# Performance work log

Measured on AMD Instinct MI355X. Metric: run time of the kernel, lower is better.

## Reference

```python
import jax, jax.numpy as jnp
import numpy as np

B, N, D = 32, 2048, 320

def _init(key, shape, fan_in):
    return jax.random.normal(key, shape, dtype=jnp.float32) / np.sqrt(fan_in).astype(np.float32)

def setup_inputs() -> dict:
    key = jax.random.key(0)
    ks = jax.random.split(key, 11)
    return {
        "x": jax.random.normal(ks[0], (B, N, D), dtype=jnp.float32),
        # downs MLP: 320->160->80
        "W1": _init(ks[1], (320, 160), 320), "b1": jnp.zeros((160,), jnp.float32),
        "W2": _init(ks[2], (160, 80), 160),  "b2": jnp.zeros((80,), jnp.float32),
        # GraphConv1d layers: 80->40, 40->5
        "Wg1": _init(ks[3], (80, 40), 80),   "bg1": jnp.zeros((40,), jnp.float32),
        "Wg2": _init(ks[4], (40, 5), 40),    "bg2": jnp.zeros((5,), jnp.float32),
        # final classifier: 5->2
        "Wf": _init(ks[5], (5, 2), 5),       "bf": jnp.zeros((2,), jnp.float32),
    }

def _euclidean_adj(h):
    # h: [B, N, C] -> row-softmax of negative squared pairwise Euclidean distance [B, N, N]
    sq = jnp.sum(h * h, axis=-1, keepdims=True)               # [B, N, 1]
    d2 = sq - 2.0 * jnp.einsum('bnc,bmc->bnm', h, h) + jnp.swapaxes(sq, -1, -2)
    return jax.nn.softmax(-d2, axis=-1)

def _graph_conv(h, W, b):
    a = _euclidean_adj(h)                                     # dynamic adjacency
    agg = jnp.einsum('bnm,bmc->bnc', a, h)                    # neighbor aggregation
    return jax.nn.relu(agg @ W + b)

def reference(x, W1, b1, W2, b2, Wg1, bg1, Wg2, bg2, Wf, bf):
    h = jax.nn.relu(x @ W1 + b1)          # [B, N, 160]
    h = jax.nn.relu(h @ W2 + b2)          # [B, N, 80]
    h = _graph_conv(h, Wg1, bg1)          # [B, N, 40]
    h = _graph_conv(h, Wg2, bg2)          # [B, N, 5]
    h = jnp.mean(h, axis=1)               # Mean() over nodes -> [B, 5]
    logits = h @ Wf + bf                  # [B, 2]
    return jax.nn.softmax(logits, axis=-1)
```

## Files before the change

kernel.cpp:

```cpp
#include <hip/hip_runtime.h>
#include <math.h>

#define BB 32
#define NN 2048
#define D_IN 320
#define H1 160
#define H2 80
#define H4 5

typedef __attribute__((ext_vector_type(8))) short short8;
typedef __attribute__((ext_vector_type(4))) short short4v;
typedef __attribute__((ext_vector_type(4))) float f32x4;
typedef __attribute__((ext_vector_type(16))) float f32x16;

__device__ inline ushort f2bf(float f) {
    union { float f; unsigned u; } v; v.f = f;
    unsigned r = v.u + 0x7fff + ((v.u >> 16) & 1);
    return (ushort)(r >> 16);
}
__device__ inline float bf2f(ushort u) {
    union { float f; unsigned u; } v; v.u = ((unsigned)u) << 16;
    return v.f;
}
__device__ inline unsigned pkbf(float hi, float lo) {
    union { float f; unsigned u; } a, b; a.f = hi; b.f = lo;
    return __builtin_amdgcn_perm(a.u + 0x8000u, b.u + 0x8000u, 0x07060302u);
}
__device__ inline float fexp2(float x) {
    float r;
    asm("v_exp_f32 %0, %1" : "=v"(r) : "v"(x));
    return r;
}
union U2S { unsigned u[2]; short4v s; };
union U4S { unsigned u[4]; short8 s; short4v h[2]; };

#define LOG2E  1.44269504088896340736f
#define TWOL2E 2.88539008177792681472f

__global__ __launch_bounds__(256) void prep_weights_kernel(
    const float* __restrict__ W1, const float* __restrict__ W2,
    const float* __restrict__ Wg1, const float* __restrict__ bg1,
    const float* __restrict__ Wg2, const float* __restrict__ bg2,
    ushort* __restrict__ Wt1, ushort* __restrict__ Wt2,
    ushort* __restrict__ Wg1B, float* __restrict__ bg1P,
    ushort* __restrict__ Wg2A, float* __restrict__ bg2P)
{
    const int id0 = blockIdx.x * 256 + threadIdx.x;
    const int stride = gridDim.x * 256;
    for (int i = id0; i < H1 * D_IN; i += stride) {
        const int j = i / D_IN, c = i % D_IN;
        Wt1[i] = f2bf(W1[c * H1 + j]);
    }
    for (int i = id0; i < H2 * H1; i += stride) {
        const int j = i / H1, c = i % H1;
        Wt2[i] = f2bf(W2[c * H2 + j]);
    }
    for (int i = id0; i < 48 * 96; i += stride) {
        const int j = i / 96, c = i % 96;
        Wg1B[i] = (j < 40 && c < 80) ? f2bf(Wg1[c * 40 + j]) : (ushort)0;
    }
    for (int i = id0; i < 32 * 48; i += stride) {
        const int j = i / 48, c = i % 48;
        const int c4 = c & 15;
        const int pos = (c & ~15) + (c4 & 3) + (((c4 >> 3) & 1) << 2) + (((c4 >> 2) & 1) << 3);
        Wg2A[j * 48 + pos] = (j < 5 && c < 40) ? f2bf(Wg2[c * 5 + j]) : (ushort)0;
    }
    if (id0 < 64) bg1P[id0] = (id0 < 40) ? bg1[id0] : 0.f;
    if (id0 < 32) bg2P[id0] = (id0 < 5) ? bg2[id0] : 0.f;
}

__global__ __launch_bounds__(256) void mlp_mfma_kernel(
    const float* __restrict__ x,
    const ushort* __restrict__ Wt1, const float* __restrict__ b1,
    const ushort* __restrict__ Wt2, const float* __restrict__ b2,
    const ushort* __restrict__ Wg1B,
    ushort* __restrict__ h2, ushort* __restrict__ V1T, float* __restrict__ sq2)
{
    constexpr int XST  = 72;
    constexpr int W1ST = 72;
    constexpr int H1ST = 168;
    constexpr int RST  = 104;

    __shared__ __attribute__((aligned(16))) ushort h1t[64 * H1ST];
    __shared__ __attribute__((aligned(16))) ushort ws1[H1 * W1ST];
    __shared__ float b1s[H1];
    __shared__ float b2s[H2];

    ushort* xs = h1t;

    const int t = threadIdx.x;
    const int lane = t & 63, w = t >> 6;
    const int colid = lane & 15, quad = lane >> 4;
    const int i = blockIdx.x;
    const int b = ((i & 7) << 2) + ((i >> 3) & 3);
    const int n0 = (i >> 5) * 64;
    const int row0 = b * NN + n0;

    if (t < H1) b1s[t] = b1[t];
    if (t < H2) b2s[t] = b2[t];

    f32x4 c1[10];
    #pragma unroll
    for (int ns = 0; ns < 10; ++ns) c1[ns] = (f32x4){0.f, 0.f, 0.f, 0.f};

    float4 xr[4];
    short8 wr[5];
    {
        #pragma unroll
        for (int i2 = 0; i2 < 4; ++i2) {
            const int id = t + i2 * 256, row = id >> 4, c4 = id & 15;
            xr[i2] = *(const float4*)&x[(size_t)(row0 + row) * D_IN + c4 * 4];
        }
        #pragma unroll
        for (int i2 = 0; i2 < 5; ++i2) {
            const int id = t + i2 * 256, j = id >> 3, part = id & 7;
            wr[i2] = *(const short8*)&Wt1[j * D_IN + part * 8];
        }
    }

    for (int kc = 0; kc < 5; ++kc) {
        if (kc) __syncthreads();
        #pragma unroll
        for (int i2 = 0; i2 < 4; ++i2) {
            const int id = t + i2 * 256, row = id >> 4, c4 = id & 15;
            uint2 up;
            up.x = pkbf(xr[i2].y, xr[i2].x);
            up.y = pkbf(xr[i2].w, xr[i2].z);
            *(uint2*)&xs[row * XST + c4 * 4] = up;
        }
        #pragma unroll
        for (int i2 = 0; i2 < 5; ++i2) {
            const int id = t + i2 * 256, j = id >> 3, part = id & 7;
            *(short8*)&ws1[j * W1ST + part * 8] = wr[i2];
        }
        __syncthreads();
        if (kc < 4) {
            const int k0 = (kc + 1) * 64;
            #pragma unroll
            for (int i2 = 0; i2 < 4; ++i2) {
                const int id = t + i2 * 256, row = id >> 4, c4 = id & 15;
                xr[i2] = *(const float4*)&x[(size_t)(row0 + row) * D_IN + k0 + c4 * 4];
            }
            #pragma unroll
            for (int i2 = 0; i2 < 5; ++i2) {
                const int id = t + i2 * 256, j = id >> 3, part = id & 7;
                wr[i2] = *(const short8*)&Wt1[j * D_IN + k0 + part * 8];
            }
        }

        short8 af[2];
        #pragma unroll
        for (int kf = 0; kf < 2; ++kf)
            af[kf] = *(const short8*)&xs[(w * 16 + colid) * XST + kf * 32 + quad * 8];
        #pragma unroll
        for (int ns = 0; ns < 10; ++ns) {
            #pragma unroll
            for (int kf = 0; kf < 2; ++kf) {
                const short8 bf = *(const short8*)&ws1[(ns * 16 + colid) * W1ST + kf * 32 + quad * 8];
                c1[ns] = __builtin_amdgcn_mfma_f32_16x16x32_bf16(af[kf], bf, c1[ns], 0, 0, 0);
            }
        }
    }
    __syncthreads();

    #pragma unroll
    for (int ns = 0; ns < 10; ++ns) {
        const float bj = b1s[ns * 16 + colid];
        #pragma unroll
        for (int r = 0; r < 4; ++r)
            h1t[(w * 16 + quad * 4 + r) * H1ST + ns * 16 + colid] =
                f2bf(fmaxf(c1[ns][r] + bj, 0.f));
    }
    __asm__ volatile("s_waitcnt lgkmcnt(0)" ::: "memory");

    short8 a2[5];
    #pragma unroll
    for (int kf = 0; kf < 5; ++kf)
        a2[kf] = *(const short8*)&h1t[(w * 16 + colid) * H1ST + kf * 32 + quad * 8];

    f32x4 c2[5];
    #pragma unroll
    for (int js = 0; js < 5; ++js) {
        f32x4 acc = (f32x4){0.f, 0.f, 0.f, 0.f};
        #pragma unroll
        for (int kf = 0; kf < 5; ++kf) {
            const short8 wb = *(const short8*)&Wt2[(js * 16 + colid) * H1 + kf * 32 + quad * 8];
            acc = __builtin_amdgcn_mfma_f32_16x16x32_bf16(a2[kf], wb, acc, 0, 0, 0);
        }
        c2[js] = acc;
    }
    __syncthreads();

    ushort* h2row = h1t;
    float rsq[4] = {0.f, 0.f, 0.f, 0.f};
    #pragma unroll
    for (int js = 0; js < 5; ++js) {
        const float bj = b2s[js * 16 + colid];
        #pragma unroll
        for (int r = 0; r < 4; ++r) {
            const ushort u = f2bf(fmaxf(c2[js][r] + bj, 0.f));
            const float vv = bf2f(u);
            rsq[r] += vv * vv;
            h2[(size_t)(row0 + w * 16 + quad * 4 + r) * 80 + js * 16 + colid] = u;
            h2row[(w * 16 + quad * 4 + r) * RST + js * 16 + colid] = u;
        }
    }
    {
        const int zr = t >> 2, zc = t & 3;
        *(short4v*)&h2row[zr * RST + 80 + zc * 4] = (short4v){0, 0, 0, 0};
    }
    __asm__ volatile("s_waitcnt lgkmcnt(0)" ::: "memory");

    short8 a3[3];
    #pragma unroll
    for (int kf = 0; kf < 3; ++kf)
        a3[kf] = *(const short8*)&h2row[(w * 16 + colid) * RST + kf * 32 + quad * 8];

    f32x4 c3[3];
    #pragma unroll
    for (int js = 0; js < 3; ++js) {
        f32x4 acc = (f32x4){0.f, 0.f, 0.f, 0.f};
        #pragma unroll
        for (int kf = 0; kf < 3; ++kf) {
            const short8 wb = *(const short8*)&Wg1B[(js * 16 + colid) * 96 + kf * 32 + quad * 8];
            acc = __builtin_amdgcn_mfma_f32_16x16x32_bf16(a3[kf], wb, acc, 0, 0, 0);
        }
        c3[js] = acc;
    }

    #pragma unroll
    for (int m = 1; m <= 8; m <<= 1)
        #pragma unroll
        for (int r = 0; r < 4; ++r) rsq[r] += __shfl_xor(rsq[r], m);
    if (colid == 0) {
        #pragma unroll
        for (int r = 0; r < 4; ++r)
            sq2[(size_t)row0 + w * 16 + quad * 4 + r] = rsq[r] * 0.5f;
    }

    ushort* Tbuf = ws1;
    #pragma unroll
    for (int js = 0; js < 3; ++js)
        #pragma unroll
        for (int r = 0; r < 4; ++r)
            Tbuf[(js * 16 + colid) * 72 + w * 16 + quad * 4 + r] = f2bf(c3[js][r]);
    __syncthreads();
    const short8 ones8 = {16256, 16256, 16256, 16256, 16256, 16256, 16256, 16256};
    for (int id = t; id < 48 * 8; id += 256) {
        const int row = id >> 3, part = id & 7;
        const short8 val = (row == 40) ? ones8 : *(const short8*)&Tbuf[row * 72 + part * 8];
        *(short8*)&V1T[((size_t)b * 48 + row) * NN + n0 + part * 8] = val;
    }
}

template<int CK, int CV, int CVS, int ONES_CH, bool HAS_OUT, bool DO_MEAN, int C_OUT>
__global__ __launch_bounds__(256, 2) void attn_conv_kernel(
    const ushort* __restrict__ h, const ushort* __restrict__ hT,
    const float* __restrict__ sqg,
    const ushort* __restrict__ WtP, const float* __restrict__ biasP,
    ushort* __restrict__ ho, ushort* __restrict__ hoT, float* __restrict__ sqo,
    float* __restrict__ mean_out)
{
    constexpr int CF   = CK / 16;
    constexpr int CSV  = CV / 32;
    constexpr int KST  = CK + 8;
    constexpr int VST  = 64 + 8;
    constexpr int KPR  = CK / 8;
    constexpr int KTOT = 64 * KPR;
    constexpr int NK   = (KTOT + 255) / 256;
    constexpr int NV   = (CV * 8) / 256;
    constexpr int TST  = 136;
    constexpr int CS1  = ONES_CH / 32;
    constexpr int R1   = ((ONES_CH % 32) / 8) * 4 + (ONES_CH & 3);
    constexpr int BUFN = 64 * KST + CV * VST;
    constexpr int NIT  = NN / 64;

    __shared__ __attribute__((aligned(16))) ushort ldsbuf[2][BUFN];
    __shared__ __attribute__((aligned(16))) float sqs[2][64];

    const int t = threadIdx.x;
    const int lane = t & 63, w = t >> 6;
    const int m32 = lane & 31, hl = lane >> 5;
    const int i = blockIdx.x;
    const int b = ((i & 7) << 2) + ((i >> 3) & 3);
    const int n0blk = (i >> 5) * 128;
    const int qrow = n0blk + w * 32 + m32;

    short8 qf[CF];
    {
        const ushort* qr = h + ((size_t)b * NN + qrow) * CK;
        #pragma unroll
        for (int c = 0; c < CF; ++c)
            qf[c] = *(const short8*)&qr[c * 16 + hl * 8];
    }
    const float nsqn = -sqg[(size_t)b * NN + qrow];

    f32x16 o[CSV];
    #pragma unroll
    for (int cs = 0; cs < CSV; ++cs)
        #pragma unroll
        for (int r = 0; r < 16; ++r) o[cs][r] = 0.f;

    short8 kreg[NK], vreg[NV];
    float sqreg = 0.f;

    auto loadTile = [&](int n1) {
        const ushort* hsrc = h + ((size_t)b * NN + n1) * CK;
        #pragma unroll
        for (int i2 = 0; i2 < NK; ++i2) {
            const int id = t + i2 * 256;
            if (KTOT % 256 == 0 || id < KTOT)
                kreg[i2] = *(const short8*)&hsrc[id * 8];
        }
        #pragma unroll
        for (int i2 = 0; i2 < NV; ++i2) {
            const int id = t + i2 * 256, c = id >> 3, pt = id & 7;
            vreg[i2] = (c < CVS)
                ? *(const short8*)&hT[((size_t)b * CVS + c) * NN + n1 + pt * 8]
                : (short8){0, 0, 0, 0, 0, 0, 0, 0};
        }
        if (t < 64) sqreg = sqg[(size_t)b * NN + n1 + t];
    };
    auto stageTile = [&](int buf) {
        ushort* Kd = ldsbuf[buf];
        ushort* Vd = ldsbuf[buf] + 64 * KST;
        #pragma unroll
        for (int i2 = 0; i2 < NK; ++i2) {
            const int id = t + i2 * 256;
            if (KTOT % 256 == 0 || id < KTOT) {
                const int row = id / KPR, pt = id % KPR;
                *(short8*)&Kd[row * KST + pt * 8] = kreg[i2];
            }
        }
        #pragma unroll
        for (int i2 = 0; i2 < NV; ++i2) {
            const int id = t + i2 * 256, c = id >> 3, pt = id & 7;
            const int colb = ((pt >> 1) << 4) + ((pt & 1) << 2);
            U4S vv; vv.s = vreg[i2];
            *(short4v*)&Vd[c * VST + colb]     = vv.h[0];
            *(short4v*)&Vd[c * VST + colb + 8] = vv.h[1];
        }
        if (t < 64) sqs[buf][t] = sqreg;
    };

    auto preloadK = [&](const ushort* Krow, short8 (&kf)[2][CF]) {
        #pragma unroll
        for (int T = 0; T < 2; ++T)
            #pragma unroll
            for (int c = 0; c < CF; ++c)
                kf[T][c] = *(const short8*)&Krow[(T * 32 + m32) * KST + c * 16 + hl * 8];
    };
    auto initST = [&](int cur, f32x16& s0, f32x16& s1) {
        #pragma unroll
        for (int g = 0; g < 4; ++g) {
            const f32x4 sm0 = *(const f32x4*)&sqs[cur][g * 8 + hl * 4];
            const f32x4 sm1 = *(const f32x4*)&sqs[cur][32 + g * 8 + hl * 4];
            #pragma unroll
            for (int r2 = 0; r2 < 4; ++r2) {
                s0[g * 4 + r2] = nsqn - sm0[r2];
                s1[g * 4 + r2] = nsqn - sm1[r2];
            }
        }
    };
    auto smfma = [&](short8 (&kf)[2][CF], f32x16& s0, f32x16& s1) {
        #pragma unroll
        for (int c = 0; c < CF; ++c) {
            s0 = __builtin_amdgcn_mfma_f32_32x32x16_bf16(kf[0][c], qf[c], s0, 0, 0, 0);
            s1 = __builtin_amdgcn_mfma_f32_32x32x16_bf16(kf[1][c], qf[c], s1, 0, 0, 0);
        }
    };
    auto preloadV = [&](const ushort* Vcol, short8 (&vf)[2][2][CSV]) {
        #pragma unroll
        for (int T = 0; T < 2; ++T)
            #pragma unroll
            for (int c = 0; c < 2; ++c)
                #pragma unroll
                for (int cs = 0; cs < CSV; ++cs)
                    vf[T][c][cs] = *(const short8*)&Vcol[(cs * 32 + m32) * VST + (T * 2 + c) * 16 + hl * 8];
    };
    auto expPV = [&](const f32x16& s0, const f32x16& s1, const short8 (&vf)[2][2][CSV]) {
        #pragma unroll
        for (int T = 0; T < 2; ++T) {
            const f32x16& st = T ? s1 : s0;
            float p[16];
            #pragma unroll
            for (int g = 0; g < 4; ++g)
                #pragma unroll
                for (int r2 = 0; r2 < 4; ++r2)
                    p[g * 4 + r2] = fexp2(st[g * 4 + r2] * TWOL2E);
            #pragma unroll
            for (int c = 0; c < 2; ++c) {
                U4S pk_;
                #pragma unroll
                for (int bq = 0; bq < 4; ++bq)
                    pk_.u[bq] = pkbf(p[c * 8 + bq * 2 + 1], p[c * 8 + bq * 2]);
                #pragma unroll
                for (int cs = 0; cs < CSV; ++cs)
                    o[cs] = __builtin_amdgcn_mfma_f32_32x32x16_bf16(vf[T][c][cs], pk_.s, o[cs], 0, 0, 0);
            }
        }
    };

    loadTile(0);
    stageTile(0);
    __syncthreads();
    loadTile(64);

    f32x16 stA0, stA1, stB0, stB1;
    short8 vfA[2][2][CSV], vfB[2][2][CSV];

    {
        short8 kf[2][CF];
        preloadK(ldsbuf[0], kf);
        initST(0, stA0, stA1);
        preloadV(ldsbuf[0] + 64 * KST, vfA);
        stageTile(1);
        loadTile(128);
        smfma(kf, stA0, stA1);
        __syncthreads();
    }

    #pragma unroll 1
    for (int k = 0; k < NIT / 2 - 1; ++k) {
        {
            short8 kf[2][CF];
            preloadK(ldsbuf[1], kf);
            initST(1, stB0, stB1);
            stageTile(0);
            loadTile((3 + 2 * k) * 64);
            smfma(kf, stB0, stB1);
            preloadV(ldsbuf[1] + 64 * KST, vfB);
            expPV(stA0, stA1, vfA);
            __syncthreads();
        }
        {
            short8 kf[2][CF];
            preloadK(ldsbuf[0], kf);
            initST(0, stA0, stA1);
            stageTile(1);
            if (k < NIT / 2 - 2) loadTile((4 + 2 * k) * 64);
            smfma(kf, stA0, stA1);
            preloadV(ldsbuf[0] + 64 * KST, vfA);
            expPV(stB0, stB1, vfB);
            __syncthreads();
        }
    }

    {
        short8 kf[2][CF];
        preloadK(ldsbuf[1], kf);
        initST(1, stB0, stB1);
        smfma(kf, stB0, stB1);
        preloadV(ldsbuf[1] + 64 * KST, vfB);
        expPV(stA0, stA1, vfA);
        __syncthreads();
    }
    expPV(stB0, stB1, vfB);

    float rsv = (hl == 0) ? o[CS1][R1] : 0.f;
    rsv += __shfl_xor(rsv, 32);
    const float rinv = 1.f / rsv;

    if constexpr (DO_MEAN) {
        float msum[4];
        #pragma unroll
        for (int r2 = 0; r2 < 4; ++r2)
            msum[r2] = fmaxf(o[0][r2] * rinv + biasP[hl * 4 + r2], 0.f);
        #pragma unroll
        for (int s = 1; s <= 16; s <<= 1)
            #pragma unroll
            for (int r2 = 0; r2 < 4; ++r2) msum[r2] += __shfl_xor(msum[r2], s);
        if (m32 == 0) {
            if (hl == 0) {
                #pragma unroll
                for (int r2 = 0; r2 < 4; ++r2)
                    atomicAdd(&mean_out[b * C_OUT + r2], msum[r2] * (1.f / NN));
            } else {
                atomicAdd(&mean_out[b * C_OUT + 4], msum[0] * (1.f / NN));
            }
        }
    }

    if constexpr (HAS_OUT) {
        float vv[CSV][16];
        float rsq = 0.f;
        #pragma unroll
        for (int cs = 0; cs < CSV; ++cs) {
            #pragma unroll
            for (int g = 0; g < 4; ++g) {
                const int jb = cs * 32 + g * 8 + hl * 4;
                const f32x4 bv = *(const f32x4*)&biasP[jb];
                float v[4];
                #pragma unroll
                for (int r2 = 0; r2 < 4; ++r2) {
                    float val = fmaxf(o[cs][g * 4 + r2] * rinv + bv[r2], 0.f);
                    if (cs == CS1 && g * 4 + r2 == R1) val = 0.f;
                    v[r2] = val;
                    vv[cs][g * 4 + r2] = val;
                }
                if (jb < 48) {
                    U2S uo;
                    uo.u[0] = pkbf(v[1], v[0]);
                    uo.u[1] = pkbf(v[3], v[2]);
                    *(short4v*)&ho[((size_t)b * NN + qrow) * 48 + jb] = uo.s;
                    #pragma unroll
                    for (int r2 = 0; r2 < 4; ++r2) {
                        const float vs = bf2f((ushort)(uo.u[r2 >> 1] >> ((r2 & 1) * 16)));
                        rsq += vs * vs;
                    }
                }
            }
        }
        const float rsq2 = rsq + __shfl_xor(rsq, 32);
        if (hl == 0) sqo[(size_t)b * NN + qrow] = rsq2 * 0.5f;

        short8 ob2[3];
        #pragma unroll
        for (int cc = 0; cc < 3; ++cc) {
            const int cs = cc >> 1, c2 = cc & 1;
            U4S ob_;
            #pragma unroll
            for (int bq = 0; bq < 4; ++bq)
                ob_.u[bq] = pkbf(vv[cs][c2 * 8 + bq * 2 + 1], vv[cs][c2 * 8 + bq * 2]);
            ob2[cc] = ob_.s;
        }
        f32x16 acc;
        #pragma unroll
        for (int r = 0; r < 16; ++r) acc[r] = 0.f;
        #pragma unroll
        for (int cc = 0; cc < 3; ++cc) {
            const short8 wa = *(const short8*)&WtP[(size_t)m32 * 48 + cc * 16 + hl * 8];
            acc = __builtin_amdgcn_mfma_f32_32x32x16_bf16(wa, ob2[cc], acc, 0, 0, 0);
        }

        ushort* Tbuf = (ushort*)ldsbuf;
        #pragma unroll
        for (int g = 0; g < 2; ++g)
            #pragma unroll
            for (int r2 = 0; r2 < 4; ++r2)
                Tbuf[(g * 8 + hl * 4 + r2) * TST + w * 32 + m32] = f2bf(acc[g * 4 + r2]);
        __syncthreads();
        const short8 ones8 = {16256, 16256, 16256, 16256, 16256, 16256, 16256, 16256};
        {
            const int row = t >> 4, part = t & 15;
            const short8 val = (row == 8) ? ones8
                             : *(const short8*)&Tbuf[row * TST + part * 8];
            *(short8*)&hoT[((size_t)b * 16 + row) * NN + n0blk + part * 8] = val;
        }
    }
}

__global__ __launch_bounds__(64) void final_kernel(
    const float* __restrict__ mean, const float* __restrict__ Wf,
    const float* __restrict__ bf, float* __restrict__ out)
{
    const int t = threadIdx.x;
    const int b = t >> 1, k = t & 1;
    float acc = bf[k];
    #pragma unroll
    for (int c = 0; c < H4; ++c) acc += mean[b * H4 + c] * Wf[c * 2 + k];
    const float other = __shfl_xor(acc, 1);
    const float mx = fmaxf(acc, other);
    const float e  = __expf(acc - mx);
    const float eo = __expf(other - mx);
    out[t] = e / (e + eo);
}

extern "C" void kernel_launch(void* const* d_in, const int* in_sizes, int n_in,
                              void* d_out, int out_size, void* d_ws, size_t ws_size,
                              hipStream_t stream) {
    const float* x   = (const float*)d_in[0];
    const float* W1  = (const float*)d_in[1];
    const float* b1  = (const float*)d_in[2];
    const float* W2  = (const float*)d_in[3];
    const float* b2  = (const float*)d_in[4];
    const float* Wg1 = (const float*)d_in[5];
    const float* bg1 = (const float*)d_in[6];
    const float* Wg2 = (const float*)d_in[7];
    const float* bg2 = (const float*)d_in[8];
    const float* Wf  = (const float*)d_in[9];
    const float* bf  = (const float*)d_in[10];

    ushort* h2   = (ushort*)d_ws;
    ushort* V1T  = h2  + (size_t)BB * NN * 80;
    float*  sq2  = (float*)(V1T + (size_t)BB * 48 * NN);
    ushort* h3   = (ushort*)(sq2 + (size_t)BB * NN);
    ushort* V2T  = h3  + (size_t)BB * NN * 48;
    float*  sq3  = (float*)(V2T + (size_t)BB * 16 * NN);
    float*  meanb = sq3 + (size_t)BB * NN;
    ushort* Wt1  = (ushort*)(meanb + 160);
    ushort* Wt2  = Wt1 + (size_t)H1 * D_IN;
    ushort* Wg1B = Wt2 + (size_t)H2 * H1;
    float*  bg1P = (float*)(Wg1B + 48 * 96);
    ushort* Wg2A = (ushort*)(bg1P + 64);
    float*  bg2P = (float*)(Wg2A + 32 * 48);

    hipMemsetAsync(meanb, 0, BB * H4 * sizeof(float), stream);

    prep_weights_kernel<<<64, 256, 0, stream>>>(W1, W2, Wg1, bg1, Wg2, bg2,
                                                Wt1, Wt2, Wg1B, bg1P, Wg2A, bg2P);
    mlp_mfma_kernel<<<BB * NN / 64, 256, 0, stream>>>(x, Wt1, b1, Wt2, b2, Wg1B,
                                                      h2, V1T, sq2);
    attn_conv_kernel<80, 64, 48, 40, true,  false, 0><<<BB * NN / 128, 256, 0, stream>>>(
        h2, V1T, sq2, Wg2A, bg1P, h3, V2T, sq3, nullptr);
    attn_conv_kernel<48, 32, 16, 8,  false, true,  5><<<BB * NN / 128, 256, 0, stream>>>(
        h3, V2T, sq3, nullptr, bg2P, nullptr, nullptr, nullptr, meanb);
    final_kernel<<<1, 64, 0, stream>>>(meanb, Wf, bf, (float*)d_out);
}
```

Baseline: 259.7 us.

## Process two KV tiles per barrier with four LDS buffers

```diff
diff --git a/kernel.cpp b/kernel.cpp
--- a/kernel.cpp
+++ b/kernel.cpp
@@ -268,15 +268,17 @@
     constexpr int KPR  = CK / 8;
     constexpr int KTOT = 64 * KPR;
     constexpr int NK   = (KTOT + 255) / 256;
-    constexpr int NV   = (CV * 8) / 256;
+    constexpr int VTOT = CVS * 8;
+    constexpr int NV   = (VTOT + 255) / 256;
     constexpr int TST  = 136;
     constexpr int CS1  = ONES_CH / 32;
     constexpr int R1   = ((ONES_CH % 32) / 8) * 4 + (ONES_CH & 3);
-    constexpr int BUFN = 64 * KST + CV * VST;
+    constexpr int BUFN = 64 * KST + CVS * VST;
     constexpr int NIT  = NN / 64;
-
-    __shared__ __attribute__((aligned(16))) ushort ldsbuf[2][BUFN];
-    __shared__ __attribute__((aligned(16))) float sqs[2][64];
+    constexpr int NRND = NIT / 2;
+
+    __shared__ __attribute__((aligned(16))) ushort ldsbuf[4][BUFN];
+    __shared__ __attribute__((aligned(16))) float sqs[4][64];
 
     const int t = threadIdx.x;
     const int lane = t & 63, w = t >> 6;
@@ -301,10 +303,10 @@
         #pragma unroll
         for (int r = 0; r < 16; ++r) o[cs][r] = 0.f;
 
-    short8 kreg[NK], vreg[NV];
-    float sqreg = 0.f;
-
-    auto loadTile = [&](int n1) {
+    short8 kregA[NK], vregA[NV]; float sqregA = 0.f;
+    short8 kregB[NK], vregB[NV]; float sqregB = 0.f;
+
+    auto loadTile = [&](int n1, short8 (&kreg)[NK], short8 (&vreg)[NV], float& sqreg) {
         const ushort* hsrc = h + ((size_t)b * NN + n1) * CK;
         #pragma unroll
         for (int i2 = 0; i2 < NK; ++i2) {
@@ -314,14 +316,15 @@
         }
         #pragma unroll
         for (int i2 = 0; i2 < NV; ++i2) {
-            const int id = t + i2 * 256, c = id >> 3, pt = id & 7;
-            vreg[i2] = (c < CVS)
-                ? *(const short8*)&hT[((size_t)b * CVS + c) * NN + n1 + pt * 8]
-                : (short8){0, 0, 0, 0, 0, 0, 0, 0};
+            const int id = t + i2 * 256;
+            if (VTOT % 256 == 0 || id < VTOT) {
+                const int c = id >> 3, pt = id & 7;
+                vreg[i2] = *(const short8*)&hT[((size_t)b * CVS + c) * NN + n1 + pt * 8];
+            }
         }
         if (t < 64) sqreg = sqg[(size_t)b * NN + n1 + t];
     };
-    auto stageTile = [&](int buf) {
+    auto stageTile = [&](int buf, const short8 (&kreg)[NK], const short8 (&vreg)[NV], float sqreg) {
         ushort* Kd = ldsbuf[buf];
         ushort* Vd = ldsbuf[buf] + 64 * KST;
         #pragma unroll
@@ -334,11 +337,14 @@
         }
         #pragma unroll
         for (int i2 = 0; i2 < NV; ++i2) {
-            const int id = t + i2 * 256, c = id >> 3, pt = id & 7;
-            const int colb = ((pt >> 1) << 4) + ((pt & 1) << 2);
-            U4S vv; vv.s = vreg[i2];
-            *(short4v*)&Vd[c * VST + colb]     = vv.h[0];
-            *(short4v*)&Vd[c * VST + colb + 8] = vv.h[1];
+            const int id = t + i2 * 256;
+            if (VTOT % 256 == 0 || id < VTOT) {
+                const int c = id >> 3, pt = id & 7;
+                const int colb = ((pt >> 1) << 4) + ((pt & 1) << 2);
+                U4S vv; vv.s = vreg[i2];
+                *(short4v*)&Vd[c * VST + colb]     = vv.h[0];
+                *(short4v*)&Vd[c * VST + colb + 8] = vv.h[1];
+            }
         }
         if (t < 64) sqs[buf][t] = sqreg;
     };
@@ -350,11 +356,11 @@
             for (int c = 0; c < CF; ++c)
                 kf[T][c] = *(const short8*)&Krow[(T * 32 + m32) * KST + c * 16 + hl * 8];
     };
-    auto initST = [&](int cur, f32x16& s0, f32x16& s1) {
+    auto initST = [&](int buf, f32x16& s0, f32x16& s1) {
         #pragma unroll
         for (int g = 0; g < 4; ++g) {
-            const f32x4 sm0 = *(const f32x4*)&sqs[cur][g * 8 + hl * 4];
-            const f32x4 sm1 = *(const f32x4*)&sqs[cur][32 + g * 8 + hl * 4];
+            const f32x4 sm0 = *(const f32x4*)&sqs[buf][g * 8 + hl * 4];
+            const f32x4 sm1 = *(const f32x4*)&sqs[buf][32 + g * 8 + hl * 4];
             #pragma unroll
             for (int r2 = 0; r2 < 4; ++r2) {
                 s0[g * 4 + r2] = nsqn - sm0[r2];
@@ -369,14 +375,19 @@
             s1 = __builtin_amdgcn_mfma_f32_32x32x16_bf16(kf[1][c], qf[c], s1, 0, 0, 0);
         }
     };
-    auto preloadV = [&](const ushort* Vcol, short8 (&vf)[2][2][CSV]) {
+    auto readV = [&](const ushort* Vcol, short8 (&vf)[2][2][CSV]) {
+        const short8 z8 = {0, 0, 0, 0, 0, 0, 0, 0};
         #pragma unroll
         for (int T = 0; T < 2; ++T)
             #pragma unroll
             for (int c = 0; c < 2; ++c)
                 #pragma unroll
-                for (int cs = 0; cs < CSV; ++cs)
-                    vf[T][c][cs] = *(const short8*)&Vcol[(cs * 32 + m32) * VST + (T * 2 + c) * 16 + hl * 8];
+                for (int cs = 0; cs < CSV; ++cs) {
+                    const int row = cs * 32 + m32;
+                    vf[T][c][cs] = (row < CVS)
+                        ? *(const short8*)&Vcol[row * VST + (T * 2 + c) * 16 + hl * 8]
+                        : z8;
+                }
     };
     auto expPV = [&](const f32x16& s0, const f32x16& s1, const short8 (&vf)[2][2][CSV]) {
         #pragma unroll
@@ -401,61 +412,47 @@
         }
     };
 
-    loadTile(0);
-    stageTile(0);
+    loadTile(0, kregA, vregA, sqregA);
+    loadTile(64, kregB, vregB, sqregB);
+    stageTile(0, kregA, vregA, sqregA);
+    stageTile(1, kregB, vregB, sqregB);
     __syncthreads();
-    loadTile(64);
-
-    f32x16 stA0, stA1, stB0, stB1;
-    short8 vfA[2][2][CSV], vfB[2][2][CSV];
-
-    {
+    loadTile(128, kregA, vregA, sqregA);
+    loadTile(192, kregB, vregB, sqregB);
+
+    #pragma unroll 1
+    for (int k = 0; k < NRND; ++k) {
+        const int p = k & 1;
+        const ushort* K0 = ldsbuf[2 * p];
+        const ushort* K1 = ldsbuf[2 * p + 1];
+
+        f32x16 s00, s01, s10, s11;
         short8 kf[2][CF];
-        preloadK(ldsbuf[0], kf);
-        initST(0, stA0, stA1);
-        preloadV(ldsbuf[0] + 64 * KST, vfA);
-        stageTile(1);
-        loadTile(128);
-        smfma(kf, stA0, stA1);
-        __syncthreads();
-    }
-
-    #pragma unroll 1
-    for (int k = 0; k < NIT / 2 - 1; ++k) {
-        {
-            short8 kf[2][CF];
-            preloadK(ldsbuf[1], kf);
-            initST(1, stB0, stB1);
-            stageTile(0);
-            loadTile((3 + 2 * k) * 64);
-            smfma(kf, stB0, stB1);
-            preloadV(ldsbuf[1] + 64 * KST, vfB);
-            expPV(stA0, stA1, vfA);
-            __syncthreads();
-        }
-        {
-            short8 kf[2][CF];
-            preloadK(ldsbuf[0], kf);
-            initST(0, stA0, stA1);
-            stageTile(1);
-            if (k < NIT / 2 - 2) loadTile((4 + 2 * k) * 64);
-            smfma(kf, stA0, stA1);
-            preloadV(ldsbuf[0] + 64 * KST, vfA);
-            expPV(stB0, stB1, vfB);
-            __syncthreads();
-        }
-    }
-
-    {
-        short8 kf[2][CF];
-        preloadK(ldsbuf[1], kf);
-        initST(1, stB0, stB1);
-        smfma(kf, stB0, stB1);
-        preloadV(ldsbuf[1] + 64 * KST, vfB);
-        expPV(stA0, stA1, vfA);
-        __syncthreads();
-    }
-    expPV(stB0, stB1, vfB);
+        preloadK(K0, kf);
+        initST(2 * p, s00, s01);
+        initST(2 * p + 1, s10, s11);
+
+        if (k < NRND - 1) {
+            stageTile(2 * (1 - p), kregA, vregA, sqregA);
+            stageTile(2 * (1 - p) + 1, kregB, vregB, sqregB);
+        }
+        if (k < NRND - 2) {
+            loadTile((2 * k + 4) * 64, kregA, vregA, sqregA);
+            loadTile((2 * k + 5) * 64, kregB, vregB, sqregB);
+        }
+
+        smfma(kf, s00, s01);
+        preloadK(K1, kf);
+        smfma(kf, s10, s11);
+
+        short8 vf[2][2][CSV];
+        readV(K0 + 64 * KST, vf);
+        expPV(s00, s01, vf);
+        readV(K1 + 64 * KST, vf);
+        expPV(s10, s11, vf);
+
+        if (k < NRND - 1) __syncthreads();
+    }
 
     float rsv = (hl == 0) ? o[CS1][R1] : 0.f;
     rsv += __shfl_xor(rsv, 32);
```

Result: slower. 265.1 us (+2.1%).
